# Optimization experiments

Measured on AMD Instinct MI355X. Metric: run time of the kernel, lower is better.

The kernel has to match this reference:

```python
import jax, jax.numpy as jnp
import numpy as np

N = 100000      # kg_E, number of entities
D = 256         # rel_dim
E = 1600000     # total COO edges (all batches concatenated)


def setup_inputs() -> dict:
    key = jax.random.key(0)
    ks = jax.random.split(key, 8)
    right_embed = jax.random.normal(ks[0], (N, D), dtype=jnp.float32)
    W1 = jax.random.normal(ks[1], (D, D), dtype=jnp.float32) * 0.02
    Wr = jax.random.normal(ks[2], (D, D), dtype=jnp.float32) * 0.02
    br = jax.random.normal(ks[3], (D,), dtype=jnp.float32) * 0.02
    edge_vals = jax.random.uniform(ks[4], (E,), dtype=jnp.float32)  # 1/(deg+1) weights
    edge_rows = jnp.sort(jax.random.randint(ks[5], (E,), 0, N))
    edge_cols = jax.random.randint(ks[6], (E,), 0, N)
    perm = jax.random.randint(ks[7], (N,), 0, N)  # ent_newid_tensor
    return {"right_embed": right_embed, "W1": W1, "Wr": Wr, "br": br,
            "edge_vals": edge_vals, "edge_rows": edge_rows,
            "edge_cols": edge_cols, "perm": perm}


def reference(right_embed, W1, Wr, br, edge_vals, edge_rows, edge_cols, perm):
    # add_diag_layer: dense transform then normalized-adjacency SpMM + ReLU
    h = right_embed @ W1                                   # [N, D]
    msg = edge_vals[:, None] * h[edge_cols]                # [E, D] gather
    agg = jax.ops.segment_sum(msg, edge_rows, num_segments=N)  # scatter-add
    gcn_e_1 = jax.nn.relu(agg)                             # [N, D]
    # highway gate blend with permuted input embeddings
    left = right_embed[perm]                               # [N, D]
    gate = jax.nn.sigmoid(left @ Wr + br)                  # [N, D]
    return gate * gcn_e_1 + (1.0 - gate) * left
```

## Files before the change

### kernel.cpp

```cpp
#include <hip/hip_runtime.h>
#include <hip/hip_bf16.h>
#include <math.h>

#define D 256

typedef short s16x8 __attribute__((ext_vector_type(8)));
typedef float f32x4 __attribute__((ext_vector_type(4)));

__device__ __forceinline__ unsigned short f2bf(float f) {
    unsigned int u = __builtin_bit_cast(unsigned int, f);
    unsigned int r = (u + 0x7fffu + ((u >> 16) & 1u)) >> 16;
    return (unsigned short)r;
}
__device__ __forceinline__ float bf2f(unsigned short s) {
    unsigned int u = ((unsigned int)s) << 16;
    return __builtin_bit_cast(float, u);
}

__global__ void swizzle_w(const float* __restrict__ W1, const float* __restrict__ Wr,
                          unsigned short* __restrict__ W1sw, unsigned short* __restrict__ Wrsw) {
    int idx = blockIdx.x * blockDim.x + threadIdx.x;
    int m = idx >> 16;
    int t = idx & 65535;
    const float* src = m ? Wr : W1;
    unsigned short* dst = m ? Wrsw : W1sw;
    int j = t & 7, lane = (t >> 3) & 63, nt = (t >> 9) & 15, kt = t >> 13;
    int k = kt * 32 + (lane >> 4) * 8 + j;
    int n = nt * 16 + (lane & 15);
    dst[t] = f2bf(src[k * D + n]);
}

__global__ void build_row_ptr(const int* __restrict__ rows, int* __restrict__ rp, int N, int E) {
    int r = blockIdx.x * blockDim.x + threadIdx.x;
    if (r > N) return;
    int lo = 0, hi = E;
    while (lo < hi) {
        int mid = (lo + hi) >> 1;
        if (rows[mid] < r) lo = mid + 1; else hi = mid;
    }
    rp[r] = lo;
}


__device__ __forceinline__ void stage_a_frag(const float* __restrict__ Xrow, int k0,
                                             unsigned short* __restrict__ lA, int fgi) {
    float4 f0 = *(const float4*)(Xrow + k0);
    float4 f1 = *(const float4*)(Xrow + k0 + 4);
    s16x8 sf;
    sf[0] = (short)f2bf(f0.x); sf[1] = (short)f2bf(f0.y);
    sf[2] = (short)f2bf(f0.z); sf[3] = (short)f2bf(f0.w);
    sf[4] = (short)f2bf(f1.x); sf[5] = (short)f2bf(f1.y);
    sf[6] = (short)f2bf(f1.z); sf[7] = (short)f2bf(f1.w);
    *(s16x8*)(lA + (size_t)fgi * 8) = sf;
}

__global__ __launch_bounds__(512) void gemm1_b(const float* __restrict__ X,
                                               const unsigned short* __restrict__ Wsw,
                                               unsigned short* __restrict__ h,
                                               int N, int numTiles) {
    __shared__ unsigned short lA[2 * 8 * 64 * 8];
    int t = threadIdx.x;
    int lane = t & 63;
    int wave = t >> 6;
    int quad = lane >> 4;

    s16x8 bfr[2][8];
#pragma unroll
    for (int ntl = 0; ntl < 2; ntl++) {
        int nt = wave * 2 + ntl;
#pragma unroll
        for (int kt = 0; kt < 8; kt++)
            bfr[ntl][kt] = *(const s16x8*)(Wsw + ((size_t)((kt * 16 + nt) * 64 + lane)) * 8);
    }

    for (int tile = blockIdx.x; tile < numTiles; tile += gridDim.x) {
#pragma unroll
        for (int q = 0; q < 2; q++) {
            int fgi = q * 512 + t;
            int mt = fgi >> 9, kt = (fgi >> 6) & 7, ll = fgi & 63;
            int rl = ll & 15, qd = ll >> 4;
            int grow = tile * 32 + mt * 16 + rl;
            if (grow >= N) grow = N - 1;
            stage_a_frag(X + (size_t)grow * D, kt * 32 + qd * 8, lA, fgi);
        }
        __syncthreads();

        f32x4 acc[2][2];
#pragma unroll
        for (int mt = 0; mt < 2; mt++)
#pragma unroll
            for (int ntl = 0; ntl < 2; ntl++) acc[mt][ntl] = (f32x4){0.f, 0.f, 0.f, 0.f};

#pragma unroll
        for (int mt = 0; mt < 2; mt++)
#pragma unroll
            for (int kt = 0; kt < 8; kt++) {
                s16x8 a = *(const s16x8*)(lA + (size_t)(((mt * 8 + kt) * 64 + lane)) * 8);
                acc[mt][0] = __builtin_amdgcn_mfma_f32_16x16x32_bf16(a, bfr[0][kt], acc[mt][0], 0, 0, 0);
                acc[mt][1] = __builtin_amdgcn_mfma_f32_16x16x32_bf16(a, bfr[1][kt], acc[mt][1], 0, 0, 0);
            }

#pragma unroll
        for (int mt = 0; mt < 2; mt++)
#pragma unroll
            for (int ntl = 0; ntl < 2; ntl++) {
                int col = (wave * 2 + ntl) * 16 + (lane & 15);
#pragma unroll
                for (int r = 0; r < 4; r++) {
                    int grow = tile * 32 + mt * 16 + quad * 4 + r;
                    if (grow < N) h[(size_t)grow * D + col] = f2bf(acc[mt][ntl][r]);
                }
            }
        __syncthreads();
    }
}

__global__ __launch_bounds__(512) void gemm2_b(const float* __restrict__ X,
                                               const int* __restrict__ perm,
                                               const unsigned short* __restrict__ Wsw,
                                               const float* __restrict__ br,
                                               const unsigned short* __restrict__ agg,
                                               float* __restrict__ out,
                                               int N, int numTiles) {
    __shared__ unsigned short lA[2 * 8 * 64 * 8];
    int t = threadIdx.x;
    int lane = t & 63;
    int wave = t >> 6;
    int quad = lane >> 4;

    s16x8 bfr[2][8];
#pragma unroll
    for (int ntl = 0; ntl < 2; ntl++) {
        int nt = wave * 2 + ntl;
#pragma unroll
        for (int kt = 0; kt < 8; kt++)
            bfr[ntl][kt] = *(const s16x8*)(Wsw + ((size_t)((kt * 16 + nt) * 64 + lane)) * 8);
    }

    for (int tile = blockIdx.x; tile < numTiles; tile += gridDim.x) {
#pragma unroll
        for (int q = 0; q < 2; q++) {
            int fgi = q * 512 + t;
            int mt = fgi >> 9, kt = (fgi >> 6) & 7, ll = fgi & 63;
            int rl = ll & 15, qd = ll >> 4;
            int grow = tile * 32 + mt * 16 + rl;
            if (grow >= N) grow = N - 1;
            int pr = perm[grow];
            stage_a_frag(X + (size_t)pr * D, kt * 32 + qd * 8, lA, fgi);
        }
        __syncthreads();

        f32x4 acc[2][2];
#pragma unroll
        for (int mt = 0; mt < 2; mt++)
#pragma unroll
            for (int ntl = 0; ntl < 2; ntl++) acc[mt][ntl] = (f32x4){0.f, 0.f, 0.f, 0.f};

#pragma unroll
        for (int mt = 0; mt < 2; mt++)
#pragma unroll
            for (int kt = 0; kt < 8; kt++) {
                s16x8 a = *(const s16x8*)(lA + (size_t)(((mt * 8 + kt) * 64 + lane)) * 8);
                acc[mt][0] = __builtin_amdgcn_mfma_f32_16x16x32_bf16(a, bfr[0][kt], acc[mt][0], 0, 0, 0);
                acc[mt][1] = __builtin_amdgcn_mfma_f32_16x16x32_bf16(a, bfr[1][kt], acc[mt][1], 0, 0, 0);
            }

#pragma unroll
        for (int mt = 0; mt < 2; mt++) {
#pragma unroll
            for (int ntl = 0; ntl < 2; ntl++) {
                int col = (wave * 2 + ntl) * 16 + (lane & 15);
                float b = br[col];
                int kt2 = col >> 5, qd2 = (col >> 3) & 3, j2 = col & 7;
#pragma unroll
                for (int r = 0; r < 4; r++) {
                    int rt = mt * 16 + quad * 4 + r;
                    int grow = tile * 32 + rt;
                    if (grow < N) {
                        float pre = acc[mt][ntl][r] + b;
                        float gate = 1.f / (1.f + __expf(-pre));
                        float gcn = bf2f(agg[(size_t)grow * D + col]);
                        float left = bf2f(lA[(size_t)(((mt * 8 + kt2) * 64 + qd2 * 16 + (rt & 15))) * 8 + j2]);
                        out[(size_t)grow * D + col] = gate * gcn + (1.f - gate) * left;
                    }
                }
            }
        }
        __syncthreads();
    }
}

__device__ __forceinline__ void acc4(float4& a, uint2 u, float v) {
    float x0 = __builtin_bit_cast(float, u.x << 16);
    float x1 = __builtin_bit_cast(float, u.x & 0xffff0000u);
    float x2 = __builtin_bit_cast(float, u.y << 16);
    float x3 = __builtin_bit_cast(float, u.y & 0xffff0000u);
    a.x += v * x0; a.y += v * x1; a.z += v * x2; a.w += v * x3;
}

__global__ __launch_bounds__(256) void scatter2(const uint2* __restrict__ hp,
                                                const int* __restrict__ rp,
                                                const int* __restrict__ cols,
                                                const float* __restrict__ vals,
                                                uint2* __restrict__ aggp,
                                                int N, int E) {
    int lane = threadIdx.x & 63;
    int wave = threadIdx.x >> 6;
    int row = blockIdx.x * 4 + wave;
    if (row >= N) return;
    int start = rp[row], end = rp[row + 1];

    float4 a = {0.f, 0.f, 0.f, 0.f};
    for (int base = start; base < end; base += 64) {
        int ii = base + lane;
        int iic = ii < E ? ii : E - 1;
        int cl = cols[iic];
        int vbits = __builtin_bit_cast(int, vals[iic]);
        int n = end - base; if (n > 64) n = 64;
        int i = 0;
        for (; i + 8 <= n; i += 8) {
            uint2 u[8]; float vv[8];
#pragma unroll
            for (int k = 0; k < 8; k++) {
                int c = __builtin_amdgcn_readlane(cl, i + k);
                vv[k] = __builtin_bit_cast(float, __builtin_amdgcn_readlane(vbits, i + k));
                u[k] = hp[(size_t)c * 64 + lane];
            }
#pragma unroll
            for (int k = 0; k < 8; k++) acc4(a, u[k], vv[k]);
        }
        for (; i < n; i++) {
            int c = __builtin_amdgcn_readlane(cl, i);
            float v = __builtin_bit_cast(float, __builtin_amdgcn_readlane(vbits, i));
            uint2 u = hp[(size_t)c * 64 + lane];
            acc4(a, u, v);
        }
    }
    a.x = fmaxf(a.x, 0.f); a.y = fmaxf(a.y, 0.f);
    a.z = fmaxf(a.z, 0.f); a.w = fmaxf(a.w, 0.f);
    uint2 o;
    o.x = (unsigned int)f2bf(a.x) | ((unsigned int)f2bf(a.y) << 16);
    o.y = (unsigned int)f2bf(a.z) | ((unsigned int)f2bf(a.w) << 16);
    aggp[(size_t)row * 64 + lane] = o;
}

extern "C" void kernel_launch(void* const* d_in, const int* in_sizes, int n_in,
                              void* d_out, int out_size, void* d_ws, size_t ws_size,
                              hipStream_t stream) {
    const float* right = (const float*)d_in[0];
    const float* W1    = (const float*)d_in[1];
    const float* Wr    = (const float*)d_in[2];
    const float* br    = (const float*)d_in[3];
    const float* evals = (const float*)d_in[4];
    const int*   erows = (const int*)d_in[5];
    const int*   ecols = (const int*)d_in[6];
    const int*   perm  = (const int*)d_in[7];
    int N = in_sizes[7];
    int E = in_sizes[4];
    float* out = (float*)d_out;

    char* ws = (char*)d_ws;
    unsigned short* W1sw = (unsigned short*)ws;
    unsigned short* Wrsw = W1sw + D * D;
    int* rp = (int*)(ws + (size_t)2 * D * D * 2);
    size_t off = (size_t)2 * D * D * 2 + 4 * (size_t)(N + 1);
    off = (off + 255) & ~(size_t)255;
    unsigned short* h = (unsigned short*)(ws + off);
    unsigned short* agg = h + (size_t)N * D;

    int numTiles = (N + 31) / 32;

    swizzle_w<<<512, 256, 0, stream>>>(W1, Wr, W1sw, Wrsw);
    build_row_ptr<<<(N + 256) / 256, 256, 0, stream>>>(erows, rp, N, E);
    gemm1_b<<<numTiles, 512, 0, stream>>>(right, W1sw, h, N, numTiles);
    scatter2<<<(N + 3) / 4, 256, 0, stream>>>((const uint2*)h, rp, ecols, evals,
                                              (uint2*)agg, N, E);
    gemm2_b<<<numTiles, 512, 0, stream>>>(right, perm, Wrsw, br, agg, out, N, numTiles);
}
```

Baseline: 417.1 us.

## Cache bf16 copy of input in gemm1 and stream it into LDS for gemm2

gemm1 now also writes a bf16 copy of right_embed to workspace. gemm2 then gathers permuted rows from that copy with global_load_lds direct-to-LDS loads, skipping the fp32 reads and per-element conversion. An fp32 fallback kernel is kept for when the workspace is too small. The scatter kernel also gains a 16-wide unrolled gather batch to raise memory-level parallelism. The extra 51 MB bf16 write in gemm1 offsets part of the read savings in gemm2.

```diff
diff --git a/kernel.cpp b/kernel.cpp
--- a/kernel.cpp
+++ b/kernel.cpp
@@ -15,6 +15,12 @@
 __device__ __forceinline__ float bf2f(unsigned short s) {
     unsigned int u = ((unsigned int)s) << 16;
     return __builtin_bit_cast(float, u);
+}
+
+__device__ __forceinline__ void gl_lds16(const void* g, void* l) {
+    __builtin_amdgcn_global_load_lds(
+        (const __attribute__((address_space(1))) void*)g,
+        (__attribute__((address_space(3))) void*)l, 16, 0, 0);
 }
 
 __global__ void swizzle_w(const float* __restrict__ W1, const float* __restrict__ Wr,
@@ -43,7 +49,8 @@
 
 
 __device__ __forceinline__ void stage_a_frag(const float* __restrict__ Xrow, int k0,
-                                             unsigned short* __restrict__ lA, int fgi) {
+                                             unsigned short* __restrict__ lA, int fgi,
+                                             s16x8* sf_out) {
     float4 f0 = *(const float4*)(Xrow + k0);
     float4 f1 = *(const float4*)(Xrow + k0 + 4);
     s16x8 sf;
@@ -52,11 +59,13 @@
     sf[4] = (short)f2bf(f1.x); sf[5] = (short)f2bf(f1.y);
     sf[6] = (short)f2bf(f1.z); sf[7] = (short)f2bf(f1.w);
     *(s16x8*)(lA + (size_t)fgi * 8) = sf;
+    *sf_out = sf;
 }
 
 __global__ __launch_bounds__(512) void gemm1_b(const float* __restrict__ X,
                                                const unsigned short* __restrict__ Wsw,
                                                unsigned short* __restrict__ h,
+                                               unsigned short* __restrict__ xbf,
                                                int N, int numTiles) {
     __shared__ unsigned short lA[2 * 8 * 64 * 8];
     int t = threadIdx.x;
@@ -81,7 +90,10 @@
             int rl = ll & 15, qd = ll >> 4;
             int grow = tile * 32 + mt * 16 + rl;
             if (grow >= N) grow = N - 1;
-            stage_a_frag(X + (size_t)grow * D, kt * 32 + qd * 8, lA, fgi);
+            int k0 = kt * 32 + qd * 8;
+            s16x8 sf;
+            stage_a_frag(X + (size_t)grow * D, k0, lA, fgi, &sf);
+            if (xbf) *(s16x8*)(xbf + (size_t)grow * D + k0) = sf;
         }
         __syncthreads();
 
@@ -115,7 +127,7 @@
     }
 }
 
-__global__ __launch_bounds__(512) void gemm2_b(const float* __restrict__ X,
+__global__ __launch_bounds__(512) void gemm2_b(const unsigned short* __restrict__ Xbf,
                                                const int* __restrict__ perm,
                                                const unsigned short* __restrict__ Wsw,
                                                const float* __restrict__ br,
@@ -140,13 +152,12 @@
     for (int tile = blockIdx.x; tile < numTiles; tile += gridDim.x) {
 #pragma unroll
         for (int q = 0; q < 2; q++) {
-            int fgi = q * 512 + t;
-            int mt = fgi >> 9, kt = (fgi >> 6) & 7, ll = fgi & 63;
-            int rl = ll & 15, qd = ll >> 4;
-            int grow = tile * 32 + mt * 16 + rl;
+            int mt = q, kt = wave;
+            int grow = tile * 32 + mt * 16 + (lane & 15);
             if (grow >= N) grow = N - 1;
             int pr = perm[grow];
-            stage_a_frag(X + (size_t)pr * D, kt * 32 + qd * 8, lA, fgi);
+            int col = kt * 32 + (lane >> 4) * 8;
+            gl_lds16(Xbf + (size_t)pr * D + col, &lA[(size_t)((mt * 8 + kt) * 64) * 8]);
         }
         __syncthreads();
 
@@ -190,6 +201,82 @@
     }
 }
 
+__global__ __launch_bounds__(512) void gemm2_fb(const float* __restrict__ X,
+                                                const int* __restrict__ perm,
+                                                const unsigned short* __restrict__ Wsw,
+                                                const float* __restrict__ br,
+                                                const unsigned short* __restrict__ agg,
+                                                float* __restrict__ out,
+                                                int N, int numTiles) {
+    __shared__ unsigned short lA[2 * 8 * 64 * 8];
+    int t = threadIdx.x;
+    int lane = t & 63;
+    int wave = t >> 6;
+    int quad = lane >> 4;
+
+    s16x8 bfr[2][8];
+#pragma unroll
+    for (int ntl = 0; ntl < 2; ntl++) {
+        int nt = wave * 2 + ntl;
+#pragma unroll
+        for (int kt = 0; kt < 8; kt++)
+            bfr[ntl][kt] = *(const s16x8*)(Wsw + ((size_t)((kt * 16 + nt) * 64 + lane)) * 8);
+    }
+
+    for (int tile = blockIdx.x; tile < numTiles; tile += gridDim.x) {
+#pragma unroll
+        for (int q = 0; q < 2; q++) {
+            int fgi = q * 512 + t;
+            int mt = fgi >> 9, kt = (fgi >> 6) & 7, ll = fgi & 63;
+            int rl = ll & 15, qd = ll >> 4;
+            int grow = tile * 32 + mt * 16 + rl;
+            if (grow >= N) grow = N - 1;
+            int pr = perm[grow];
+            s16x8 sf;
+            stage_a_frag(X + (size_t)pr * D, kt * 32 + qd * 8, lA, fgi, &sf);
+        }
+        __syncthreads();
+
+        f32x4 acc[2][2];
+#pragma unroll
+        for (int mt = 0; mt < 2; mt++)
+#pragma unroll
+            for (int ntl = 0; ntl < 2; ntl++) acc[mt][ntl] = (f32x4){0.f, 0.f, 0.f, 0.f};
+
+#pragma unroll
+        for (int mt = 0; mt < 2; mt++)
+#pragma unroll
+            for (int kt = 0; kt < 8; kt++) {
+                s16x8 a = *(const s16x8*)(lA + (size_t)(((mt * 8 + kt) * 64 + lane)) * 8);
+                acc[mt][0] = __builtin_amdgcn_mfma_f32_16x16x32_bf16(a, bfr[0][kt], acc[mt][0], 0, 0, 0);
+                acc[mt][1] = __builtin_amdgcn_mfma_f32_16x16x32_bf16(a, bfr[1][kt], acc[mt][1], 0, 0, 0);
+            }
+
+#pragma unroll
+        for (int mt = 0; mt < 2; mt++) {
+#pragma unroll
+            for (int ntl = 0; ntl < 2; ntl++) {
+                int col = (wave * 2 + ntl) * 16 + (lane & 15);
+                float b = br[col];
+                int kt2 = col >> 5, qd2 = (col >> 3) & 3, j2 = col & 7;
+#pragma unroll
+                for (int r = 0; r < 4; r++) {
+                    int rt = mt * 16 + quad * 4 + r;
+                    int grow = tile * 32 + rt;
+                    if (grow < N) {
+                        float pre = acc[mt][ntl][r] + b;
+                        float gate = 1.f / (1.f + __expf(-pre));
+                        float gcn = bf2f(agg[(size_t)grow * D + col]);
+                        float left = bf2f(lA[(size_t)(((mt * 8 + kt2) * 64 + qd2 * 16 + (rt & 15))) * 8 + j2]);
+                        out[(size_t)grow * D + col] = gate * gcn + (1.f - gate) * left;
+                    }
+                }
+            }
+        }
+        __syncthreads();
+    }
+}
+
 __device__ __forceinline__ void acc4(float4& a, uint2 u, float v) {
     float x0 = __builtin_bit_cast(float, u.x << 16);
     float x1 = __builtin_bit_cast(float, u.x & 0xffff0000u);
@@ -218,6 +305,17 @@
         int vbits = __builtin_bit_cast(int, vals[iic]);
         int n = end - base; if (n > 64) n = 64;
         int i = 0;
+        for (; i + 16 <= n; i += 16) {
+            uint2 u[16]; float vv[16];
+#pragma unroll
+            for (int k = 0; k < 16; k++) {
+                int c = __builtin_amdgcn_readlane(cl, i + k);
+                vv[k] = __builtin_bit_cast(float, __builtin_amdgcn_readlane(vbits, i + k));
+                u[k] = hp[(size_t)c * 64 + lane];
+            }
+#pragma unroll
+            for (int k = 0; k < 16; k++) acc4(a, u[k], vv[k]);
+        }
         for (; i + 8 <= n; i += 8) {
             uint2 u[8]; float vv[8];
 #pragma unroll
@@ -267,13 +365,18 @@
     off = (off + 255) & ~(size_t)255;
     unsigned short* h = (unsigned short*)(ws + off);
     unsigned short* agg = h + (size_t)N * D;
+    unsigned short* xbf = agg + (size_t)N * D;
+    bool fast = ws_size >= off + 3 * (size_t)N * D * 2;
 
     int numTiles = (N + 31) / 32;
 
     swizzle_w<<<512, 256, 0, stream>>>(W1, Wr, W1sw, Wrsw);
     build_row_ptr<<<(N + 256) / 256, 256, 0, stream>>>(erows, rp, N, E);
-    gemm1_b<<<numTiles, 512, 0, stream>>>(right, W1sw, h, N, numTiles);
+    gemm1_b<<<numTiles, 512, 0, stream>>>(right, W1sw, h, fast ? xbf : nullptr, N, numTiles);
     scatter2<<<(N + 3) / 4, 256, 0, stream>>>((const uint2*)h, rp, ecols, evals,
                                               (uint2*)agg, N, E);
-    gemm2_b<<<numTiles, 512, 0, stream>>>(right, perm, Wrsw, br, agg, out, N, numTiles);
-}
+    if (fast)
+        gemm2_b<<<numTiles, 512, 0, stream>>>(xbf, perm, Wrsw, br, agg, out, N, numTiles);
+    else
+        gemm2_fb<<<numTiles, 512, 0, stream>>>(right, perm, Wrsw, br, agg, out, N, numTiles);
+}
```

Result: no change. 418.4 us (+0.3%).
